# Optimization experiments

Hardware: AMD Instinct MI355X
Metric: run time of the kernel (lower is better)

## Reference

```python
import jax, jax.numpy as jnp
import numpy as np

B, L, D, H = 2, 4096, 1024, 4
DV = D // H
NP = 5
MIN_PROB = 0.01
CHUNK = 32
RIN = D + H * NP * 4 + H * (NP * (NP - 1)) // 2  # 1144
RH = 2 * RIN


def dwconv_causal(x, w):
    # x: (B, L, C); w: (C, K) depthwise causal FIR
    K = w.shape[-1]
    xp = jnp.pad(x, ((0, 0), (K - 1, 0), (0, 0))).transpose(0, 2, 1)  # (B,C,L+K-1)
    y = jax.lax.conv_general_dilated(
        xp, w[:, None, :], window_strides=(1,), padding='VALID',
        feature_group_count=w.shape[0],
        dimension_numbers=('NCH', 'OIH', 'NCH'))
    return y.transpose(0, 2, 1)  # (B,L,C)


def l2norm(x):
    return x * jax.lax.rsqrt(jnp.sum(x * x, -1, keepdims=True) + 1e-12)


def delta_rule_chunkwise(q, k, v, beta, chunk=CHUNK):
    # q,k: (b,h,L,dk)  v: (b,h,L,dv)  beta: (b,h,L); L divisible by chunk
    b, h, Lq, dk = q.shape
    dv = v.shape[-1]
    n = Lq // chunk
    q = l2norm(q); k = l2norm(k)
    v = v * beta[..., None]
    kb = k * beta[..., None]
    r = lambda x: x.reshape(b, h, n, chunk, -1)
    q, k, v, kb = r(q), r(k), r(v), r(kb)
    tri = jnp.triu(jnp.ones((chunk, chunk), bool), 0)
    attn = jnp.where(tri, 0.0, -(kb @ jnp.swapaxes(k, -1, -2)))
    for i in range(1, chunk):  # in-chunk triangular-inverse recurrence
        upd = jnp.einsum('...k,...ki->...i', attn[..., i, :], attn[..., :, :i])
        attn = attn.at[..., i, :i].add(upd)
    attn = attn + jnp.eye(chunk, dtype=attn.dtype)
    u = attn @ v
    w = attn @ kb
    strict = jnp.triu(jnp.ones((chunk, chunk), bool), 1)

    def step(S, inp):
        qi, ki, ui, wi = inp
        la = jnp.where(strict, 0.0, qi @ jnp.swapaxes(ki, -1, -2))
        u_i = ui - wi @ S
        o_i = qi @ S + la @ u_i
        return S + jnp.swapaxes(ki, -1, -2) @ u_i, o_i

    mv = lambda x: jnp.moveaxis(x, 2, 0)
    S0 = jnp.zeros((b, h, dk, dv), q.dtype)
    S, o = jax.lax.scan(step, S0, (mv(q), mv(k), mv(u), mv(w)))
    return jnp.moveaxis(o, 0, 2).reshape(b, h, Lq, dv), S


def setup_inputs() -> dict:
    key = jax.random.key(0)
    ks = jax.random.split(key, 20)
    f = lambda k, shape, s=0.02: jax.random.normal(k, shape, jnp.float32) * s
    # FIR filters: identity tap (last) + small noise, matching learned-from-delta init
    def fir(k, ksz):
        w = np.zeros((D, ksz), np.float32)
        w[:, -1] = 1.0
        return jnp.asarray(w) + f(k, (D, ksz), 0.02)
    b2 = np.zeros((H, NP), np.float32)
    b2[:, -1] = 0.5
    b2[:, -2] = 0.5
    return {
        'hidden_states': jax.random.normal(ks[0], (B, L, D), jnp.float32),
        'Wq': f(ks[1], (D, D)), 'Wk': f(ks[2], (D, D)), 'Wv': f(ks[3], (D, D)),
        'wq_conv': f(ks[4], (D, 4), 0.2), 'wk_conv': f(ks[5], (D, 4), 0.2),
        'wv_conv': f(ks[6], (D, 4), 0.2),
        'Wb': f(ks[7], (H, D)),
        'fir_s_w': fir(ks[8], 3), 'fir_m_w': fir(ks[9], 7),
        'fir_l_w': fir(ks[10], 25), 'fir_id_w': fir(ks[11], 1),
        'W1': f(ks[12], (RH, RIN)), 'b1': jnp.zeros((RH,), jnp.float32),
        'W2': f(ks[13], (H * NP, RH)), 'b2': jnp.asarray(b2.reshape(-1)),
        'norm_w': jnp.ones((DV,), jnp.float32),
        'Wo': f(ks[14], (D, D)),
    }


def reference(hidden_states, Wq, Wk, Wv, wq_conv, wk_conv, wv_conv, Wb,
              fir_s_w, fir_m_w, fir_l_w, fir_id_w, W1, b1, W2, b2, norm_w, Wo):
    silu = jax.nn.silu
    q = silu(dwconv_causal(hidden_states @ Wq.T, wq_conv))
    k = silu(dwconv_causal(hidden_states @ Wk.T, wk_conv))
    v = silu(dwconv_causal(hidden_states @ Wv.T, wv_conv))
    beta = jax.nn.sigmoid(hidden_states @ Wb.T)  # (B,L,H)
    q4 = q.reshape(B, L, H, -1).transpose(0, 2, 1, 3)
    k4 = k.reshape(B, L, H, -1).transpose(0, 2, 1, 3)
    v4 = v.reshape(B, L, H, -1).transpose(0, 2, 1, 3)
    delta_out, _ = delta_rule_chunkwise(q4, k4, v4, beta.transpose(0, 2, 1))
    delta_out = delta_out.transpose(0, 2, 1, 3)  # (B,L,H,DV)
    fir = lambda w: dwconv_causal(v, w).reshape(B, L, H, DV)
    branches = [fir(fir_s_w), fir(fir_m_w), fir(fir_l_w), delta_out, fir(fir_id_w)]
    feats = []
    for x in branches:
        sm = jax.nn.softmax(x, -1)
        feats += [x.mean(-1), jnp.var(x, -1, ddof=1), jnp.max(x, -1),
                  -(sm * jnp.log(sm + 1e-8)).sum(-1)]
    cross = []
    for i in range(NP):
        for j in range(i + 1, NP):
            xi, xj = branches[i], branches[j]
            den = jnp.sqrt(jnp.sum(xi * xi, -1)) * jnp.sqrt(jnp.sum(xj * xj, -1)) + 1e-8
            cross.append(jnp.sum(xi * xj, -1) / den)
    router_in = jnp.concatenate([hidden_states] + feats + cross, axis=-1)  # (B,L,RIN)
    hrt = jax.nn.gelu(router_in @ W1.T + b1, approximate=False)
    logits = (hrt @ W2.T + b2).reshape(B, L, H, NP)
    p = jax.nn.softmax(logits, -1)
    p = p * (1.0 - NP * MIN_PROB) + MIN_PROB  # probability floor
    out = jnp.einsum('blhp,pblhd->blhd', p, jnp.stack(branches))
    out = out * jax.lax.rsqrt(jnp.mean(out * out, -1, keepdims=True) + 1e-5) * norm_w
    return out.reshape(B, L, H * DV) @ Wo.T
```

## Files before the change

### kernel.cpp

```cpp
#include <hip/hip_runtime.h>
#include <stdint.h>

typedef unsigned short u16t;
typedef u16t us4 __attribute__((ext_vector_type(4)));
typedef u16t us8 __attribute__((ext_vector_type(8)));
typedef __bf16 bf8v __attribute__((ext_vector_type(8)));
typedef float f4 __attribute__((ext_vector_type(4)));

#define MFMA(a, b, c) __builtin_amdgcn_mfma_f32_16x16x32_bf16((a), (b), (c), 0, 0, 0)

__device__ __forceinline__ float bf2f(u16t u) {
  union { unsigned int i; float f; } c; c.i = ((unsigned int)u) << 16; return c.f;
}
__device__ __forceinline__ u16t f2bf(float f) {
  union { float f; unsigned int i; } c; c.f = f;
  return (u16t)((c.i + 0x7FFFu + ((c.i >> 16) & 1u)) >> 16);
}
__device__ __forceinline__ float wsum(float v) {
#pragma unroll
  for (int o = 32; o > 0; o >>= 1) v += __shfl_xor(v, o);
  return v;
}
__device__ __forceinline__ float wmax(float v) {
#pragma unroll
  for (int o = 32; o > 0; o >>= 1) v = fmaxf(v, __shfl_xor(v, o));
  return v;
}

__global__ __launch_bounds__(256) void pack_bf16(const float* __restrict__ src,
    u16t* __restrict__ dst, int n4) {
  const int i = blockIdx.x * 256 + threadIdx.x;
  if (i >= n4) return;
  f4 v = *(const f4*)&src[(size_t)i * 4];
  us4 o;
#pragma unroll
  for (int e = 0; e < 4; ++e) o[e] = f2bf(v[e]);
  *(us4*)&dst[(size_t)i * 4] = o;
}

template <bool AF32, bool BF32, bool CF32>
__device__ __forceinline__ void gemm_body(const void* __restrict__ Av,
    const void* __restrict__ Btv, void* __restrict__ Cv,
    int K, int lda, int ldb, int ldc, int m0, int n0) {
  __shared__ u16t As[128][40];
  __shared__ u16t Bs[128][40];
  const int tid = threadIdx.x;
  const int wv = tid >> 6, l = tid & 63;
  const int wr = wv >> 1, wc = wv & 1;
  const int lr = l & 15, kg8 = (l >> 4) * 8, rg4 = (l >> 4) * 4;
  const int row_s = tid >> 1, seg = (tid & 1) * 16;
  const f4 zf = {0.f, 0.f, 0.f, 0.f};
  f4 acc[4][4];
#pragma unroll
  for (int i = 0; i < 4; ++i)
#pragma unroll
    for (int j = 0; j < 4; ++j) acc[i][j] = zf;

  for (int kt = 0; kt < K; kt += 32) {
    us8 a0, a1, b0, b1;
    if (AF32) {
      const float* pa = (const float*)Av + (size_t)(m0 + row_s) * lda + seg + kt;
      f4 fa0 = *(const f4*)(pa), fa1 = *(const f4*)(pa + 4);
      f4 fa2 = *(const f4*)(pa + 8), fa3 = *(const f4*)(pa + 12);
#pragma unroll
      for (int e = 0; e < 4; ++e) {
// ... 21 lines not shown
    *(us8*)&As[row_s][seg + 8] = a1;
    *(us8*)&Bs[row_s][seg] = b0;
    *(us8*)&Bs[row_s][seg + 8] = b1;
    __syncthreads();
    bf8v af[4], bg[4];
#pragma unroll
    for (int f = 0; f < 4; ++f) af[f] = *(const bf8v*)&As[wr * 64 + f * 16 + lr][kg8];
#pragma unroll
    for (int f = 0; f < 4; ++f) bg[f] = *(const bf8v*)&Bs[wc * 64 + f * 16 + lr][kg8];
#pragma unroll
    for (int i = 0; i < 4; ++i)
#pragma unroll
      for (int j = 0; j < 4; ++j) acc[i][j] = MFMA(af[i], bg[j], acc[i][j]);
    __syncthreads();
  }
#pragma unroll
  for (int i = 0; i < 4; ++i) {
    const int rb = m0 + wr * 64 + i * 16 + rg4;
#pragma unroll
    for (int j = 0; j < 4; ++j) {
      const int cb = n0 + wc * 64 + j * 16 + lr;
#pragma unroll
      for (int r = 0; r < 4; ++r) {
        if (CF32)
          ((float*)Cv)[(size_t)(rb + r) * ldc + cb] = acc[i][j][r];
        else
          ((u16t*)Cv)[(size_t)(rb + r) * ldc + cb] = f2bf(acc[i][j][r]);
      }
    }
  }
}

template <bool AF32, bool BF32, bool CF32>
__global__ __launch_bounds__(256) void gemm_bt(const void* __restrict__ Av,
    const void* __restrict__ Btv, void* __restrict__ Cv,
    int K, int lda, int ldb, int ldc) {
  gemm_body<AF32, BF32, CF32>(Av, Btv, Cv, K, lda, ldb, ldc,
                              blockIdx.y * 128, blockIdx.x * 128);
}

__global__ __launch_bounds__(256) void gemm_qkv3(const u16t* __restrict__ A,
    const u16t* __restrict__ B0, const u16t* __restrict__ B1,
    const u16t* __restrict__ B2, u16t* __restrict__ C0, u16t* __restrict__ C1,
    u16t* __restrict__ C2v) {
  const int z = blockIdx.z;
  const u16t* Bt = (z == 0) ? B0 : ((z == 1) ? B1 : B2);
  u16t* C = (z == 0) ? C0 : ((z == 1) ? C1 : C2v);
  gemm_body<false, false, false>(A, Bt, C, 1024, 1024, 1024, 1024,
                                 blockIdx.y * 128, blockIdx.x * 128);
}

__global__ __launch_bounds__(256) void conv4_silu(
    const u16t* __restrict__ qlin, const u16t* __restrict__ klin, const u16t* __restrict__ vlin,
    const float* __restrict__ wq, const float* __restrict__ wk, const float* __restrict__ wvv,
    u16t* __restrict__ qc, u16t* __restrict__ kc, u16t* __restrict__ vc) {
  const int tid = threadIdx.x;
  const int l0 = blockIdx.x * 64;
  const int b = blockIdx.y >> 2, cb = blockIdx.y & 3;
  const int z = blockIdx.z;
  const u16t* in_ = (z == 0) ? qlin : ((z == 1) ? klin : vlin);
  const float* w_ = (z == 0) ? wq : ((z == 1) ? wk : wvv);
  u16t* out_ = (z == 0) ? qc : ((z == 1) ? kc : vc);
  const int c = cb * 256 + tid;
  __shared__ u16t sm[67][256];
  for (int i = 0; i < 67; ++i) {
    int ls = l0 - 3 + i;
    sm[i][tid] = (ls >= 0) ? in_[((size_t)b * 4096 + ls) * 1024 + c] : (u16t)0;
  }
  __syncthreads();
  f4 w4 = *(const f4*)&w_[c * 4];
  float x0 = bf2f(sm[0][tid]), x1 = bf2f(sm[1][tid]), x2 = bf2f(sm[2][tid]);
  for (int ll = 0; ll < 64; ++ll) {
    float x3 = bf2f(sm[ll + 3][tid]);
    float y = x0 * w4[0] + x1 * w4[1] + x2 * w4[2] + x3 * w4[3];
    y = y / (1.f + expf(-y));
    out_[((size_t)b * 4096 + l0 + ll) * 1024 + c] = f2bf(y);
    x0 = x1; x1 = x2; x2 = x3;
  }
}

__global__ __launch_bounds__(256) void beta_kernel(const float* __restrict__ hid,
    const float* __restrict__ Wb, float* __restrict__ beta) {
  const int m = blockIdx.x, tid = threadIdx.x;
  const int h = tid >> 6, l = tid & 63;
  float acc = 0.f;
#pragma unroll
  for (int it = 0; it < 4; ++it) {
    int kk = l * 4 + it * 256;
    f4 hv = *(const f4*)&hid[(size_t)m * 1024 + kk];
    f4 wv4 = *(const f4*)&Wb[(size_t)h * 1024 + kk];
#pragma unroll
    for (int e = 0; e < 4; ++e) acc += hv[e] * wv4[e];
  }
  acc = wsum(acc);
  if (l == 0) beta[m * 4 + h] = 1.f / (1.f + expf(-acc));
}

__global__ __launch_bounds__(256) void prep_kernel(u16t* __restrict__ qc, u16t* __restrict__ kc,
    const u16t* __restrict__ vc, const float* __restrict__ beta,
    u16t* __restrict__ kbeta, u16t* __restrict__ vbeta) {
  const int m = blockIdx.x, tid = threadIdx.x;
  const int h = tid >> 6, l = tid & 63;
  const size_t base = (size_t)m * 1024 + h * 256 + l * 4;
  const float bet = beta[m * 4 + h];
  us4 q4 = *(const us4*)&qc[base];
  float qf[4]; float ss = 0.f;
#pragma unroll
  for (int e = 0; e < 4; ++e) { qf[e] = bf2f(q4[e]); ss += qf[e] * qf[e]; }
  float qsc = rsqrtf(wsum(ss) + 1e-12f);
  us4 qo;
#pragma unroll
  for (int e = 0; e < 4; ++e) qo[e] = f2bf(qf[e] * qsc);
  *(us4*)&qc[base] = qo;
  us4 k4 = *(const us4*)&kc[base];
  float kf[4]; ss = 0.f;
#pragma unroll
  for (int e = 0; e < 4; ++e) { kf[e] = bf2f(k4[e]); ss += kf[e] * kf[e]; }
  float ksc = rsqrtf(wsum(ss) + 1e-12f);
  us4 ko, kbo;
#pragma unroll
  for (int e = 0; e < 4; ++e) {
    float kn = kf[e] * ksc;
    ko[e] = f2bf(kn);
    kbo[e] = f2bf(kn * bet);
  }
  *(us4*)&kc[base] = ko;
  *(us4*)&kbeta[base] = kbo;
// ... 74 lines not shown
        us8 v8 = *(const us8*)&vbs[j][cg + e0];
        us8 k8 = *(const us8*)&kbs[j][cg + e0];
#pragma unroll
        for (int e = 0; e < 8; ++e) {
          ua[e0 + e] += a * bf2f(v8[e]);
          wa[e0 + e] += a * bf2f(k8[e]);
        }
      }
    }
    const size_t ob = ((size_t)bh * 4096 + l0 + r) * 256 + cg;
#pragma unroll
    for (int e0 = 0; e0 < 32; e0 += 8) {
      us8 pu, pw;
#pragma unroll
      for (int e = 0; e < 8; ++e) { pu[e] = f2bf(ua[e0 + e]); pw[e] = f2bf(wa[e0 + e]); }
      *(us8*)&ug[ob + e0] = pu;
      *(us8*)&wg[ob + e0] = pw;
    }
  }
}

__global__ __launch_bounds__(256, 1) void delta_scan(const u16t* __restrict__ qn,
    const u16t* __restrict__ kn, const u16t* __restrict__ ug, const u16t* __restrict__ wg,
    u16t* __restrict__ dout) {
  const int blk = blockIdx.x;
  const int bh = blk >> 2, vbidx = blk & 3;
  const int b = bh >> 2, h = bh & 3;
  const int c0 = vbidx * 64;
  const int tid = threadIdx.x;
  const int wv = tid >> 6, l = tid & 63;
  const int lr = l & 15, kg8 = (l >> 4) * 8, rg4 = (l >> 4) * 4;

  __shared__ u16t qs[32][264], ks2[32][264], wss[32][264];
  __shared__ u16t kts[256][40];
  __shared__ u16t sbf[64][264];
  __shared__ u16t las[32][40];
  __shared__ u16t uts[64][40];

  {
    u16t* sp = &sbf[0][0];
    for (int i = tid; i < 64 * 264; i += 256) sp[i] = 0;
  }
  const f4 zf = {0.f, 0.f, 0.f, 0.f};
  f4 sacc[16];
#pragma unroll
  for (int d = 0; d < 16; ++d) sacc[d] = zf;
  __syncthreads();

  const u16t* qb = qn + (size_t)b * 4096 * 1024 + (size_t)h * 256;
  const u16t* knb = kn + (size_t)b * 4096 * 1024 + (size_t)h * 256;
  const u16t* ub = ug + (size_t)bh * 4096 * 256;
  const u16t* wb = wg + (size_t)bh * 4096 * 256;
  const int sr = tid >> 5, sd8 = (tid & 31) * 8;

  us8 pq[4], pk[4], pw[4];
  us4 pu0, pu1;
  {
#pragma unroll
    for (int i = 0; i < 4; ++i) {
      const int r = i * 8 + sr;
      pq[i] = *(const us8*)(qb + (size_t)r * 1024 + sd8);
      pk[i] = *(const us8*)(knb + (size_t)r * 1024 + sd8);
      pw[i] = *(const us8*)(wb + (size_t)r * 256 + sd8);
    }
    pu0 = *(const us4*)(ub + (size_t)lr * 256 + c0 + wv * 16 + rg4);
    pu1 = *(const us4*)(ub + (size_t)(16 + lr) * 256 + c0 + wv * 16 + rg4);
  }

  for (int ci = 0; ci < 128; ++ci) {
    const int l0 = ci * 32;
#pragma unroll
    for (int i = 0; i < 4; ++i) {
      const int r = i * 8 + sr;
      *(us8*)&qs[r][sd8] = pq[i];
      *(us8*)&ks2[r][sd8] = pk[i];
      *(us8*)&wss[r][sd8] = pw[i];
    }
    const us4 u0 = pu0, u1 = pu1;
    __syncthreads();
    if (ci < 127) {
      const int l1 = l0 + 32;
#pragma unroll
      for (int i = 0; i < 4; ++i) {
        const int r = i * 8 + sr;
        pq[i] = *(const us8*)(qb + (size_t)(l1 + r) * 1024 + sd8);
        pk[i] = *(const us8*)(knb + (size_t)(l1 + r) * 1024 + sd8);
        pw[i] = *(const us8*)(wb + (size_t)(l1 + r) * 256 + sd8);
      }
      pu0 = *(const us4*)(ub + (size_t)(l1 + lr) * 256 + c0 + wv * 16 + rg4);
      pu1 = *(const us4*)(ub + (size_t)(l1 + 16 + lr) * 256 + c0 + wv * 16 + rg4);
    }
    {
      const int dk = tid;
      const int swz = ((dk >> 3) & 3) << 3;
#pragma unroll
      for (int r = 0; r < 32; r += 2) {
        unsigned int lo = ks2[r][dk], hi = ks2[r + 1][dk];
        *(unsigned int*)&kts[dk][r ^ swz] = lo | (hi << 16);
      }
    }
    {
      const int rq = wv >> 1, rk = wv & 1;
      f4 t4 = zf;
#pragma unroll
      for (int ks = 0; ks < 8; ++ks) {
        bf8v a = *(const bf8v*)&qs[rq * 16 + lr][ks * 32 + kg8];
        bf8v bb = *(const bf8v*)&ks2[rk * 16 + lr][ks * 32 + kg8];
        t4 = MFMA(a, bb, t4);
      }
      const int colj = rk * 16 + lr;
#pragma unroll
      for (int rr = 0; rr < 4; ++rr) {
        const int rowr = rq * 16 + rg4 + rr;
        las[rowr][colj] = (colj <= rowr) ? f2bf(t4[rr]) : (u16t)0;
      }
    }
    f4 o0 = zf, o1 = zf;
    {
      f4 m0 = zf, m1 = zf;
#pragma unroll
      for (int ks = 0; ks < 8; ++ks) {
        bf8v a = *(const bf8v*)&sbf[wv * 16 + lr][ks * 32 + kg8];
        bf8v wb0 = *(const bf8v*)&wss[lr][ks * 32 + kg8];
        bf8v wb1 = *(const bf8v*)&wss[16 + lr][ks * 32 + kg8];
        bf8v qb0 = *(const bf8v*)&qs[lr][ks * 32 + kg8];
        bf8v qb1 = *(const bf8v*)&qs[16 + lr][ks * 32 + kg8];
        m0 = MFMA(a, wb0, m0);
        m1 = MFMA(a, wb1, m1);
        o0 = MFMA(a, qb0, o0);
        o1 = MFMA(a, qb1, o1);
      }
#pragma unroll
      for (int rt = 0; rt < 2; ++rt) {
        f4 mm = rt ? m1 : m0;
        const us4 uu = rt ? u1 : u0;
        const int r = rt * 16 + lr;
#pragma unroll
        for (int rr = 0; rr < 4; ++rr)
          uts[wv * 16 + rg4 + rr][r] = f2bf(bf2f(uu[rr]) - mm[rr]);
      }
    }
    __syncthreads();
    {
      bf8v a2 = *(const bf8v*)&uts[wv * 16 + lr][kg8];
      {
        bf8v lb0 = *(const bf8v*)&las[lr][kg8];
        bf8v lb1 = *(const bf8v*)&las[16 + lr][kg8];
        o0 = MFMA(a2, lb0, o0);
        o1 = MFMA(a2, lb1, o1);
      }
#pragma unroll
      for (int rt = 0; rt < 2; ++rt) {
        f4 oo = rt ? o1 : o0;
        const int r = rt * 16 + lr;
        us4 st;
#pragma unroll
        for (int rr = 0; rr < 4; ++rr) st[rr] = f2bf(oo[rr]);
        *(us4*)(dout + ((size_t)(b * 4096 + l0 + r) * 4 + h) * 256 + c0 + wv * 16 + rg4) = st;
      }
#pragma unroll
      for (int d = 0; d < 16; ++d) {
        const int swzd = ((2 * d + (lr >> 3)) & 3) << 3;
        bf8v bb = *(const bf8v*)&kts[d * 16 + lr][kg8 ^ swzd];
        sacc[d] = MFMA(a2, bb, sacc[d]);
      }
#pragma unroll
      for (int d = 0; d < 16; ++d) {
#pragma unroll
        for (int rr = 0; rr < 4; ++rr)
          sbf[wv * 16 + rg4 + rr][d * 16 + lr] = f2bf(sacc[d][rr]);
      }
    }
    __syncthreads();
  }
}

__global__ __launch_bounds__(256) void fir_kernel(const u16t* __restrict__ vc,
    const float* __restrict__ w3g, const float* __restrict__ w7g,
    const float* __restrict__ w25g, const float* __restrict__ w1g,
    u16t* __restrict__ fs, u16t* __restrict__ fm, u16t* __restrict__ fl,
    u16t* __restrict__ fid) {
  const int tid = threadIdx.x;
  const int l0 = blockIdx.x * 64;
  const int b = blockIdx.y >> 2, cb = blockIdx.y & 3;
  const int c = cb * 256 + tid;
  __shared__ u16t sm[88][256];
  for (int i = 0; i < 88; ++i) {
    int ls = l0 - 24 + i;
    sm[i][tid] = (ls >= 0) ? vc[((size_t)b * 4096 + ls) * 1024 + c] : (u16t)0;
  }
  __syncthreads();
  float w3[3], w7[7], w25[25], w1_;
#pragma unroll
  for (int j = 0; j < 3; ++j) w3[j] = w3g[c * 3 + j];
#pragma unroll
  for (int j = 0; j < 7; ++j) w7[j] = w7g[c * 7 + j];
#pragma unroll
  for (int j = 0; j < 25; ++j) w25[j] = w25g[c * 25 + j];
  w1_ = w1g[c];
  float x[25];
#pragma unroll
  for (int j = 0; j < 25; ++j) x[j] = bf2f(sm[j][tid]);
  for (int ll = 0; ll < 64; ++ll) {
    float ys = x[22] * w3[0] + x[23] * w3[1] + x[24] * w3[2];
    float ym = 0.f;
#pragma unroll
    for (int j = 0; j < 7; ++j) ym += x[18 + j] * w7[j];
    float yl = 0.f;
#pragma unroll
    for (int j = 0; j < 25; ++j) yl += x[j] * w25[j];
    float yi = x[24] * w1_;
    const size_t o = ((size_t)b * 4096 + l0 + ll) * 1024 + c;
    fs[o] = f2bf(ys); fm[o] = f2bf(ym); fl[o] = f2bf(yl); fid[o] = f2bf(yi);
    if (ll < 63) {
#pragma unroll
      for (int j = 0; j < 24; ++j) x[j] = x[j + 1];
      x[24] = bf2f(sm[ll + 25][tid]);
    }
  }
}

__global__ __launch_bounds__(256) void features_kernel(const float* __restrict__ hid,
    const u16t* __restrict__ p0, const u16t* __restrict__ p1, const u16t* __restrict__ p2,
    const u16t* __restrict__ p3, const u16t* __restrict__ p4, u16t* __restrict__ router) {
  const int m = blockIdx.x, tid = threadIdx.x;
  const int h = tid >> 6, l = tid & 63;
  const size_t base = (size_t)m * 1024 + h * 256 + l * 4;
  const u16t* bp[5] = {p0, p1, p2, p3, p4};
  float x[5][4];
#pragma unroll
  for (int br = 0; br < 5; ++br) {
    us4 v = *(const us4*)&bp[br][base];
#pragma unroll
    for (int e = 0; e < 4; ++e) x[br][e] = bf2f(v[e]);
  }
  float s1[5], s2[5], mx[5];
#pragma unroll
  for (int br = 0; br < 5; ++br) {
    float a = 0.f, bq = 0.f, m_ = -1e30f;
#pragma unroll
    for (int e = 0; e < 4; ++e) {
      a += x[br][e]; bq += x[br][e] * x[br][e]; m_ = fmaxf(m_, x[br][e]);
    }
    s1[br] = wsum(a); s2[br] = wsum(bq); mx[br] = wmax(m_);
  }
  float ent[5];
#pragma unroll
  for (int br = 0; br < 5; ++br) {
    float e_ = 0.f;
#pragma unroll
    for (int e = 0; e < 4; ++e) e_ += expf(x[br][e] - mx[br]);
    float es = wsum(e_);
    float hn = 0.f;
#pragma unroll
    for (int e = 0; e < 4; ++e) {
      float pv = expf(x[br][e] - mx[br]) / es;
      hn += pv * logf(pv + 1e-8f);
// ... 25 lines not shown
      rp[br * 16 + 8 + h] = f2bf(mx[br]);
      rp[br * 16 + 12 + h] = f2bf(ent[br]);
    }
    int pi = 0;
#pragma unroll
    for (int i = 0; i < 5; ++i)
#pragma unroll
      for (int j = i + 1; j < 5; ++j) {
        float den = sqrtf(s2[i]) * sqrtf(s2[j]) + 1e-8f;
        rp[80 + pi * 4 + h] = f2bf(dt[pi] / den);
        ++pi;
      }
  }
  {
    f4 hv = *(const f4*)&hid[(size_t)m * 1024 + tid * 4];
    us4 hv4;
#pragma unroll
    for (int e = 0; e < 4; ++e) hv4[e] = f2bf(hv[e]);
    *(us4*)&router[(size_t)m * 1152 + tid * 4] = hv4;
  }
  if (tid < 8) router[(size_t)m * 1152 + 1144 + tid] = 0;
}

__global__ __launch_bounds__(256) void gelu_bias(u16t* __restrict__ hrt,
    const float* __restrict__ b1) {
  const size_t idx = ((size_t)blockIdx.x * 256 + threadIdx.x) * 4;
  const int col = (int)(idx % 2304);
  us4 v = *(const us4*)&hrt[idx];
  us4 o;
#pragma unroll
  for (int e = 0; e < 4; ++e) {
    int cc = col + e;
    float xx = bf2f(v[e]) + ((cc < 2288) ? b1[cc] : 0.f);
    float g = 0.5f * xx * (1.f + erff(xx * 0.70710678118f));
    o[e] = f2bf(g);
  }
  *(us4*)&hrt[idx] = o;
}

__global__ __launch_bounds__(256) void w2_softmax(const u16t* __restrict__ hrt,
    const float* __restrict__ W2, const float* __restrict__ b2, float* __restrict__ pout) {
  const int m = blockIdx.x, tid = threadIdx.x;
  const int h = tid >> 6, l = tid & 63;
  float acc[5];
#pragma unroll
  for (int n = 0; n < 5; ++n) acc[n] = 0.f;
  for (int kk = l * 4; kk < 2288; kk += 256) {
    us4 hv = *(const us4*)&hrt[(size_t)m * 2304 + kk];
    float hf[4];
#pragma unroll
    for (int e = 0; e < 4; ++e) hf[e] = bf2f(hv[e]);
#pragma unroll
    for (int n = 0; n < 5; ++n) {
      f4 wv4 = *(const f4*)&W2[(size_t)(h * 5 + n) * 2288 + kk];
#pragma unroll
      for (int e = 0; e < 4; ++e) acc[n] += hf[e] * wv4[e];
    }
  }
#pragma unroll
  for (int n = 0; n < 5; ++n) acc[n] = wsum(acc[n]);
  if (l == 0) {
    float lg[5];
#pragma unroll
    for (int n = 0; n < 5; ++n) lg[n] = acc[n] + b2[h * 5 + n];
    float mxv = lg[0];
#pragma unroll
    for (int n = 1; n < 5; ++n) mxv = fmaxf(mxv, lg[n]);
    float es = 0.f, ev[5];
#pragma unroll
    for (int n = 0; n < 5; ++n) { ev[n] = expf(lg[n] - mxv); es += ev[n]; }
#pragma unroll
    for (int n = 0; n < 5; ++n)
      pout[(size_t)m * 20 + h * 5 + n] = (ev[n] / es) * 0.95f + 0.01f;
  }
}

__global__ __launch_bounds__(256) void mix_kernel(const u16t* __restrict__ p0,
    const u16t* __restrict__ p1, const u16t* __restrict__ p2, const u16t* __restrict__ p3,
    const u16t* __restrict__ p4, const float* __restrict__ pbuf,
    const float* __restrict__ normw, u16t* __restrict__ mixed) {
  const int m = blockIdx.x, tid = threadIdx.x;
  const int h = tid >> 6, l = tid & 63;
  const size_t base = (size_t)m * 1024 + h * 256 + l * 4;
  const u16t* bp[5] = {p0, p1, p2, p3, p4};
  float p5[5];
#pragma unroll
  for (int n = 0; n < 5; ++n) p5[n] = pbuf[(size_t)m * 20 + h * 5 + n];
  float o[4] = {0.f, 0.f, 0.f, 0.f};
#pragma unroll
  for (int br = 0; br < 5; ++br) {
    us4 v = *(const us4*)&bp[br][base];
#pragma unroll
    for (int e = 0; e < 4; ++e) o[e] += p5[br] * bf2f(v[e]);
  }
  float ss = 0.f;
#pragma unroll
  for (int e = 0; e < 4; ++e) ss += o[e] * o[e];
  ss = wsum(ss);
  float sc = rsqrtf(ss * (1.f / 256.f) + 1e-5f);
  f4 nw = *(const f4*)&normw[l * 4];
  us4 ov;
#pragma unroll
  for (int e = 0; e < 4; ++e) ov[e] = f2bf(o[e] * sc * nw[e]);
  *(us4*)&mixed[base] = ov;
}

__global__ __launch_bounds__(256) void pad_w1(const float* __restrict__ W1,
    u16t* __restrict__ W1p) {
  size_t idx = (size_t)blockIdx.x * 256 + threadIdx.x;
  if (idx >= (size_t)2304 * 1152) return;
  int n = (int)(idx / 1152), k = (int)(idx % 1152);
  W1p[idx] = (n < 2288 && k < 1144) ? f2bf(W1[(size_t)n * 1144 + k]) : (u16t)0;
}

extern "C" void kernel_launch(void* const* d_in, const int* in_sizes, int n_in,
                              void* d_out, int out_size, void* d_ws, size_t ws_size,
                              hipStream_t stream) {
  (void)in_sizes; (void)n_in; (void)out_size; (void)ws_size;
  const float* hid = (const float*)d_in[0];
  const float* Wq = (const float*)d_in[1];
  const float* Wk = (const float*)d_in[2];
  const float* Wv = (const float*)d_in[3];
  const float* wqc = (const float*)d_in[4];
  const float* wkc = (const float*)d_in[5];
  const float* wvc = (const float*)d_in[6];
  const float* Wb = (const float*)d_in[7];
  const float* fsw = (const float*)d_in[8];
  const float* fmw = (const float*)d_in[9];
  const float* flw = (const float*)d_in[10];
  const float* fiw = (const float*)d_in[11];
  const float* W1 = (const float*)d_in[12];
  const float* b1 = (const float*)d_in[13];
  const float* W2 = (const float*)d_in[14];
  const float* b2 = (const float*)d_in[15];
  const float* nwt = (const float*)d_in[16];
  const float* Wo = (const float*)d_in[17];
  float* out = (float*)d_out;

  char* wsp = (char*)d_ws;
  const size_t S = (size_t)2 * 4096 * 1024 * 2;
  u16t* ql = (u16t*)(wsp + 0 * S);
  u16t* kl = (u16t*)(wsp + 1 * S);
  u16t* vl = (u16t*)(wsp + 2 * S);
  u16t* qc = (u16t*)(wsp + 3 * S);
  u16t* kc = (u16t*)(wsp + 4 * S);
  u16t* vc = (u16t*)(wsp + 5 * S);
  u16t* ubuf = (u16t*)(wsp + 6 * S);
  u16t* wbuf = (u16t*)(wsp + 7 * S);
  char* p = wsp + 8 * S;
  u16t* router = (u16t*)p; p += (size_t)8192 * 1152 * 2;
  u16t* hrt = (u16t*)p;    p += (size_t)8192 * 2304 * 2;
  u16t* w1p = (u16t*)p;    p += (size_t)2304 * 1152 * 2;
  float* pbuf = (float*)p; p += (size_t)8192 * 20 * 4;
  float* beta = (float*)p; p += (size_t)8192 * 4 * 4;
  u16t* hidb = qc;
  u16t* wqb = kc;
  u16t* wkb = kc + 1048576;
  u16t* wvb = kc + 2097152;
  u16t* kbeta = ql;
  u16t* vbeta = kl;
  u16t* dlt = kl;
  u16t* f_s = vl;
  u16t* f_m = qc;
  u16t* f_l = kc;
  u16t* f_i = ubuf;
  u16t* mixed = wbuf;
  u16t* wob = w1p;

  dim3 blk(256);
  pack_bf16<<<dim3(8192), blk, 0, stream>>>(hid, hidb, 2097152);
  pack_bf16<<<dim3(1024), blk, 0, stream>>>(Wq, wqb, 262144);
  pack_bf16<<<dim3(1024), blk, 0, stream>>>(Wk, wkb, 262144);
  pack_bf16<<<dim3(1024), blk, 0, stream>>>(Wv, wvb, 262144);
  gemm_qkv3<<<dim3(8, 64, 3), blk, 0, stream>>>(hidb, wqb, wkb, wvb, ql, kl, vl);
  conv4_silu<<<dim3(64, 8, 3), blk, 0, stream>>>(ql, kl, vl, wqc, wkc, wvc, qc, kc, vc);
  beta_kernel<<<dim3(8192), blk, 0, stream>>>(hid, Wb, beta);
  prep_kernel<<<dim3(8192), blk, 0, stream>>>(qc, kc, vc, beta, kbeta, vbeta);
  chunk_uw<<<dim3(1024), blk, 0, stream>>>(kc, kbeta, vbeta, ubuf, wbuf);
  delta_scan<<<dim3(32), blk, 0, stream>>>(qc, kc, ubuf, wbuf, dlt);
  fir_kernel<<<dim3(64, 8), blk, 0, stream>>>(vc, fsw, fmw, flw, fiw, f_s, f_m, f_l, f_i);
  features_kernel<<<dim3(8192), blk, 0, stream>>>(hid, f_s, f_m, f_l, dlt, f_i, router);
  pad_w1<<<dim3(10368), blk, 0, stream>>>(W1, w1p);
  gemm_bt<false, false, false><<<dim3(18, 64), blk, 0, stream>>>(router, w1p, hrt, 1152, 1152, 1152, 2304);
  gelu_bias<<<dim3(18432), blk, 0, stream>>>(hrt, b1);
  w2_softmax<<<dim3(8192), blk, 0, stream>>>(hrt, W2, b2, pbuf);
  mix_kernel<<<dim3(8192), blk, 0, stream>>>(f_s, f_m, f_l, dlt, f_i, pbuf, nwt, mixed);
  pack_bf16<<<dim3(1024), blk, 0, stream>>>(Wo, wob, 262144);
  gemm_bt<false, false, true><<<dim3(8, 64), blk, 0, stream>>>(mixed, wob, out, 1024, 1024, 1024, 1024);
}
```

Measured before the change: 1.099 ms.

## Fuse packs, beta, gelu epilogue; overlap FIR and W1 pad with delta scan

Merges the four fp32-to-bf16 pack launches into one, folds beta computation into prep_kernel, and moves bias+GELU into the W1 GEMM epilogue, removing a full pass over hrt. The 32-block delta_scan launch now also carries extra blocks that compute the 25-tap FIR and pad W1, so that work uses otherwise idle CUs during the serial scan. Short FIRs (3, 7, identity) are recomputed on the fly in features and mix kernels instead of being stored. The cost is a larger delta_scan kernel with more shared memory and a risk of register and occupancy pressure, plus redundant FIR recompute in two kernels.

```diff
diff --git a/kernel.cpp b/kernel.cpp
--- a/kernel.cpp
+++ b/kernel.cpp
@@ -25,6 +25,23 @@
 #pragma unroll
   for (int o = 32; o > 0; o >>= 1) v = fmaxf(v, __shfl_xor(v, o));
   return v;
+}
+
+__global__ __launch_bounds__(256) void pack_all(const float* __restrict__ hid,
+    const float* __restrict__ Wq, const float* __restrict__ Wk, const float* __restrict__ Wv,
+    u16t* __restrict__ hidb, u16t* __restrict__ wqb, u16t* __restrict__ wkb,
+    u16t* __restrict__ wvb) {
+  const int g = blockIdx.x * 256 + threadIdx.x;
+  const float* src; u16t* dst; int off;
+  if (g < 2097152) { src = hid; dst = hidb; off = g; }
+  else if (g < 2359296) { src = Wq; dst = wqb; off = g - 2097152; }
+  else if (g < 2621440) { src = Wk; dst = wkb; off = g - 2359296; }
+  else { src = Wv; dst = wvb; off = g - 2621440; }
+  f4 v = *(const f4*)&src[(size_t)off * 4];
+  us4 o;
+#pragma unroll
+  for (int e = 0; e < 4; ++e) o[e] = f2bf(v[e]);
+  *(us4*)&dst[(size_t)off * 4] = o;
 }
 
 __global__ __launch_bounds__(256) void pack_bf16(const float* __restrict__ src,
@@ -38,9 +55,9 @@
   *(us4*)&dst[(size_t)i * 4] = o;
 }
 
-template <bool AF32, bool BF32, bool CF32>
+template <bool AF32, bool BF32, bool CF32, int EPI>
 __device__ __forceinline__ void gemm_body(const void* __restrict__ Av,
-    const void* __restrict__ Btv, void* __restrict__ Cv,
+    const void* __restrict__ Btv, void* __restrict__ Cv, const float* __restrict__ bias,
     int K, int lda, int ldb, int ldc, int m0, int n0) {
   __shared__ u16t As[128][40];
   __shared__ u16t Bs[128][40];
@@ -108,21 +125,26 @@
       const int cb = n0 + wc * 64 + j * 16 + lr;
 #pragma unroll
       for (int r = 0; r < 4; ++r) {
+        float x = acc[i][j][r];
+        if (EPI == 1) {
+          float xx = x + ((cb < 2288) ? bias[cb] : 0.f);
+          x = 0.5f * xx * (1.f + erff(xx * 0.70710678118f));
+        }
         if (CF32)
-          ((float*)Cv)[(size_t)(rb + r) * ldc + cb] = acc[i][j][r];
+          ((float*)Cv)[(size_t)(rb + r) * ldc + cb] = x;
         else
-          ((u16t*)Cv)[(size_t)(rb + r) * ldc + cb] = f2bf(acc[i][j][r]);
-      }
-    }
-  }
-}
-
-template <bool AF32, bool BF32, bool CF32>
+          ((u16t*)Cv)[(size_t)(rb + r) * ldc + cb] = f2bf(x);
+      }
+    }
+  }
+}
+
+template <bool AF32, bool BF32, bool CF32, int EPI>
 __global__ __launch_bounds__(256) void gemm_bt(const void* __restrict__ Av,
-    const void* __restrict__ Btv, void* __restrict__ Cv,
+    const void* __restrict__ Btv, void* __restrict__ Cv, const float* __restrict__ bias,
     int K, int lda, int ldb, int ldc) {
-  gemm_body<AF32, BF32, CF32>(Av, Btv, Cv, K, lda, ldb, ldc,
-                              blockIdx.y * 128, blockIdx.x * 128);
+  gemm_body<AF32, BF32, CF32, EPI>(Av, Btv, Cv, bias, K, lda, ldb, ldc,
+                                   blockIdx.y * 128, blockIdx.x * 128);
 }
 
 __global__ __launch_bounds__(256) void gemm_qkv3(const u16t* __restrict__ A,
@@ -132,8 +154,8 @@
   const int z = blockIdx.z;
   const u16t* Bt = (z == 0) ? B0 : ((z == 1) ? B1 : B2);
   u16t* C = (z == 0) ? C0 : ((z == 1) ? C1 : C2v);
-  gemm_body<false, false, false>(A, Bt, C, 1024, 1024, 1024, 1024,
-                                 blockIdx.y * 128, blockIdx.x * 128);
+  gemm_body<false, false, false, 0>(A, Bt, C, nullptr, 1024, 1024, 1024, 1024,
+                                    blockIdx.y * 128, blockIdx.x * 128);
 }
 
 __global__ __launch_bounds__(256) void conv4_silu(
@@ -165,30 +187,22 @@
   }
 }
 
-__global__ __launch_bounds__(256) void beta_kernel(const float* __restrict__ hid,
-    const float* __restrict__ Wb, float* __restrict__ beta) {
+__global__ __launch_bounds__(256) void prep_kernel(u16t* __restrict__ qc, u16t* __restrict__ kc,
+    const u16t* __restrict__ vc, const float* __restrict__ hid, const float* __restrict__ Wb,
+    u16t* __restrict__ kbeta, u16t* __restrict__ vbeta) {
   const int m = blockIdx.x, tid = threadIdx.x;
   const int h = tid >> 6, l = tid & 63;
-  float acc = 0.f;
+  float bacc = 0.f;
 #pragma unroll
   for (int it = 0; it < 4; ++it) {
     int kk = l * 4 + it * 256;
     f4 hv = *(const f4*)&hid[(size_t)m * 1024 + kk];
     f4 wv4 = *(const f4*)&Wb[(size_t)h * 1024 + kk];
 #pragma unroll
-    for (int e = 0; e < 4; ++e) acc += hv[e] * wv4[e];
-  }
-  acc = wsum(acc);
-  if (l == 0) beta[m * 4 + h] = 1.f / (1.f + expf(-acc));
-}
-
-__global__ __launch_bounds__(256) void prep_kernel(u16t* __restrict__ qc, u16t* __restrict__ kc,
-    const u16t* __restrict__ vc, const float* __restrict__ beta,
-    u16t* __restrict__ kbeta, u16t* __restrict__ vbeta) {
-  const int m = blockIdx.x, tid = threadIdx.x;
-  const int h = tid >> 6, l = tid & 63;
+    for (int e = 0; e < 4; ++e) bacc += hv[e] * wv4[e];
+  }
+  const float bet = 1.f / (1.f + expf(-wsum(bacc)));
   const size_t base = (size_t)m * 1024 + h * 256 + l * 4;
-  const float bet = beta[m * 4 + h];
   us4 q4 = *(const us4*)&qc[base];
   float qf[4]; float ss = 0.f;
 #pragma unroll
@@ -309,40 +323,41 @@
 
 __global__ __launch_bounds__(256, 1) void delta_scan(const u16t* __restrict__ qn,
     const u16t* __restrict__ kn, const u16t* __restrict__ ug, const u16t* __restrict__ wg,
-    u16t* __restrict__ dout) {
+    u16t* __restrict__ dout, const u16t* __restrict__ vc, const float* __restrict__ w25g,
+    u16t* __restrict__ fl, const float* __restrict__ W1, u16t* __restrict__ W1p) {
   const int blk = blockIdx.x;
-  const int bh = blk >> 2, vbidx = blk & 3;
-  const int b = bh >> 2, h = bh & 3;
-  const int c0 = vbidx * 64;
   const int tid = threadIdx.x;
-  const int wv = tid >> 6, l = tid & 63;
-  const int lr = l & 15, kg8 = (l >> 4) * 8, rg4 = (l >> 4) * 4;
-
-  __shared__ u16t qs[32][264], ks2[32][264], wss[32][264];
-  __shared__ u16t kts[256][40];
-  __shared__ u16t sbf[64][264];
-  __shared__ u16t las[32][40];
-  __shared__ u16t uts[64][40];
-
-  {
-    u16t* sp = &sbf[0][0];
-    for (int i = tid; i < 64 * 264; i += 256) sp[i] = 0;
-  }
-  const f4 zf = {0.f, 0.f, 0.f, 0.f};
-  f4 sacc[16];
-#pragma unroll
-  for (int d = 0; d < 16; ++d) sacc[d] = zf;
-  __syncthreads();
-
-  const u16t* qb = qn + (size_t)b * 4096 * 1024 + (size_t)h * 256;
-  const u16t* knb = kn + (size_t)b * 4096 * 1024 + (size_t)h * 256;
-  const u16t* ub = ug + (size_t)bh * 4096 * 256;
-  const u16t* wb = wg + (size_t)bh * 4096 * 256;
-  const int sr = tid >> 5, sd8 = (tid & 31) * 8;
-
-  us8 pq[4], pk[4], pw[4];
-  us4 pu0, pu1;
-  {
+  if (blk < 32) {
+    const int bh = blk >> 2, vbidx = blk & 3;
+    const int b = bh >> 2, h = bh & 3;
+    const int c0 = vbidx * 64;
+    const int wv = tid >> 6, l = tid & 63;
+    const int lr = l & 15, kg8 = (l >> 4) * 8, rg4 = (l >> 4) * 4;
+
+    __shared__ u16t qs[32][264], ks2[32][264], wss[32][264];
+    __shared__ u16t kts[256][40];
+    __shared__ u16t sbf[64][264];
+    __shared__ u16t las[32][40];
+    __shared__ u16t uts[64][40];
+
+    {
+      u16t* sp = &sbf[0][0];
+      for (int i = tid; i < 64 * 264; i += 256) sp[i] = 0;
+    }
+    const f4 zf = {0.f, 0.f, 0.f, 0.f};
+    f4 sacc[16];
+#pragma unroll
+    for (int d = 0; d < 16; ++d) sacc[d] = zf;
+    __syncthreads();
+
+    const u16t* qb = qn + (size_t)b * 4096 * 1024 + (size_t)h * 256;
+    const u16t* knb = kn + (size_t)b * 4096 * 1024 + (size_t)h * 256;
+    const u16t* ub = ug + (size_t)bh * 4096 * 256;
+    const u16t* wb = wg + (size_t)bh * 4096 * 256;
+    const int sr = tid >> 5, sd8 = (tid & 31) * 8;
+
+    us8 pq[4], pk[4], pw[4];
+    us4 pu0, pu1;
 #pragma unroll
     for (int i = 0; i < 4; ++i) {
       const int r = i * 8 + sr;
@@ -352,174 +367,198 @@
     }
     pu0 = *(const us4*)(ub + (size_t)lr * 256 + c0 + wv * 16 + rg4);
     pu1 = *(const us4*)(ub + (size_t)(16 + lr) * 256 + c0 + wv * 16 + rg4);
-  }
-
-  for (int ci = 0; ci < 128; ++ci) {
-    const int l0 = ci * 32;
-#pragma unroll
-    for (int i = 0; i < 4; ++i) {
-      const int r = i * 8 + sr;
-      *(us8*)&qs[r][sd8] = pq[i];
-      *(us8*)&ks2[r][sd8] = pk[i];
-      *(us8*)&wss[r][sd8] = pw[i];
-    }
-    const us4 u0 = pu0, u1 = pu1;
-    __syncthreads();
-    if (ci < 127) {
-      const int l1 = l0 + 32;
+
+    for (int ci = 0; ci < 128; ++ci) {
+      const int l0 = ci * 32;
 #pragma unroll
       for (int i = 0; i < 4; ++i) {
         const int r = i * 8 + sr;
-        pq[i] = *(const us8*)(qb + (size_t)(l1 + r) * 1024 + sd8);
-        pk[i] = *(const us8*)(knb + (size_t)(l1 + r) * 1024 + sd8);
-        pw[i] = *(const us8*)(wb + (size_t)(l1 + r) * 256 + sd8);
-      }
-      pu0 = *(const us4*)(ub + (size_t)(l1 + lr) * 256 + c0 + wv * 16 + rg4);
-      pu1 = *(const us4*)(ub + (size_t)(l1 + 16 + lr) * 256 + c0 + wv * 16 + rg4);
-    }
-    {
-      const int dk = tid;
-      const int swz = ((dk >> 3) & 3) << 3;
-#pragma unroll
-      for (int r = 0; r < 32; r += 2) {
-        unsigned int lo = ks2[r][dk], hi = ks2[r + 1][dk];
-        *(unsigned int*)&kts[dk][r ^ swz] = lo | (hi << 16);
-      }
-    }
-    {
-      const int rq = wv >> 1, rk = wv & 1;
-      f4 t4 = zf;
-#pragma unroll
-      for (int ks = 0; ks < 8; ++ks) {
-        bf8v a = *(const bf8v*)&qs[rq * 16 + lr][ks * 32 + kg8];
-        bf8v bb = *(const bf8v*)&ks2[rk * 16 + lr][ks * 32 + kg8];
-        t4 = MFMA(a, bb, t4);
-      }
-      const int colj = rk * 16 + lr;
-#pragma unroll
-      for (int rr = 0; rr < 4; ++rr) {
-        const int rowr = rq * 16 + rg4 + rr;
-        las[rowr][colj] = (colj <= rowr) ? f2bf(t4[rr]) : (u16t)0;
-      }
-    }
-    f4 o0 = zf, o1 = zf;
-    {
-      f4 m0 = zf, m1 = zf;
-#pragma unroll
-      for (int ks = 0; ks < 8; ++ks) {
-        bf8v a = *(const bf8v*)&sbf[wv * 16 + lr][ks * 32 + kg8];
-        bf8v wb0 = *(const bf8v*)&wss[lr][ks * 32 + kg8];
-        bf8v wb1 = *(const bf8v*)&wss[16 + lr][ks * 32 + kg8];
-        bf8v qb0 = *(const bf8v*)&qs[lr][ks * 32 + kg8];
-        bf8v qb1 = *(const bf8v*)&qs[16 + lr][ks * 32 + kg8];
-        m0 = MFMA(a, wb0, m0);
-        m1 = MFMA(a, wb1, m1);
-        o0 = MFMA(a, qb0, o0);
-        o1 = MFMA(a, qb1, o1);
-      }
-#pragma unroll
-      for (int rt = 0; rt < 2; ++rt) {
-        f4 mm = rt ? m1 : m0;
-        const us4 uu = rt ? u1 : u0;
-        const int r = rt * 16 + lr;
-#pragma unroll
-        for (int rr = 0; rr < 4; ++rr)
-          uts[wv * 16 + rg4 + rr][r] = f2bf(bf2f(uu[rr]) - mm[rr]);
-      }
+        *(us8*)&qs[r][sd8] = pq[i];
+        *(us8*)&ks2[r][sd8] = pk[i];
+        *(us8*)&wss[r][sd8] = pw[i];
+      }
+      const us4 u0 = pu0, u1 = pu1;
+      __syncthreads();
+      if (ci < 127) {
+        const int l1 = l0 + 32;
+#pragma unroll
+        for (int i = 0; i < 4; ++i) {
+          const int r = i * 8 + sr;
+          pq[i] = *(const us8*)(qb + (size_t)(l1 + r) * 1024 + sd8);
+          pk[i] = *(const us8*)(knb + (size_t)(l1 + r) * 1024 + sd8);
+          pw[i] = *(const us8*)(wb + (size_t)(l1 + r) * 256 + sd8);
+        }
+        pu0 = *(const us4*)(ub + (size_t)(l1 + lr) * 256 + c0 + wv * 16 + rg4);
+        pu1 = *(const us4*)(ub + (size_t)(l1 + 16 + lr) * 256 + c0 + wv * 16 + rg4);
+      }
+      {
+        const int dk = tid;
+        const int swz = ((dk >> 3) & 3) << 3;
+#pragma unroll
+        for (int r = 0; r < 32; r += 2) {
+          unsigned int lo = ks2[r][dk], hi = ks2[r + 1][dk];
+          *(unsigned int*)&kts[dk][r ^ swz] = lo | (hi << 16);
+        }
+      }
+      {
+        const int rq = wv >> 1, rk = wv & 1;
+        f4 t4 = zf;
+#pragma unroll
+        for (int ks = 0; ks < 8; ++ks) {
+          bf8v a = *(const bf8v*)&qs[rq * 16 + lr][ks * 32 + kg8];
+          bf8v bb = *(const bf8v*)&ks2[rk * 16 + lr][ks * 32 + kg8];
+          t4 = MFMA(a, bb, t4);
+        }
+        const int colj = rk * 16 + lr;
+#pragma unroll
+        for (int rr = 0; rr < 4; ++rr) {
+          const int rowr = rq * 16 + rg4 + rr;
+          las[rowr][colj] = (colj <= rowr) ? f2bf(t4[rr]) : (u16t)0;
+        }
+      }
+      f4 o0 = zf, o1 = zf;
+      {
+        f4 m0 = zf, m1 = zf;
+#pragma unroll
+        for (int ks = 0; ks < 8; ++ks) {
+          bf8v a = *(const bf8v*)&sbf[wv * 16 + lr][ks * 32 + kg8];
+          bf8v wb0 = *(const bf8v*)&wss[lr][ks * 32 + kg8];
+          bf8v wb1 = *(const bf8v*)&wss[16 + lr][ks * 32 + kg8];
+          bf8v qb0 = *(const bf8v*)&qs[lr][ks * 32 + kg8];
+          bf8v qb1 = *(const bf8v*)&qs[16 + lr][ks * 32 + kg8];
+          m0 = MFMA(a, wb0, m0);
+          m1 = MFMA(a, wb1, m1);
+          o0 = MFMA(a, qb0, o0);
+          o1 = MFMA(a, qb1, o1);
+        }
+#pragma unroll
+        for (int rt = 0; rt < 2; ++rt) {
+          f4 mm = rt ? m1 : m0;
+          const us4 uu = rt ? u1 : u0;
+          const int r = rt * 16 + lr;
+#pragma unroll
+          for (int rr = 0; rr < 4; ++rr)
+            uts[wv * 16 + rg4 + rr][r] = f2bf(bf2f(uu[rr]) - mm[rr]);
+        }
+      }
+      __syncthreads();
+      {
+        bf8v a2 = *(const bf8v*)&uts[wv * 16 + lr][kg8];
+        {
+          bf8v lb0 = *(const bf8v*)&las[lr][kg8];
+          bf8v lb1 = *(const bf8v*)&las[16 + lr][kg8];
+          o0 = MFMA(a2, lb0, o0);
+          o1 = MFMA(a2, lb1, o1);
+        }
+#pragma unroll
+        for (int rt = 0; rt < 2; ++rt) {
+          f4 oo = rt ? o1 : o0;
+          const int r = rt * 16 + lr;
+          us4 st;
+#pragma unroll
+          for (int rr = 0; rr < 4; ++rr) st[rr] = f2bf(oo[rr]);
+          *(us4*)(dout + ((size_t)(b * 4096 + l0 + r) * 4 + h) * 256 + c0 + wv * 16 + rg4) = st;
+        }
+#pragma unroll
+        for (int d = 0; d < 16; ++d) {
+          const int swzd = ((2 * d + (lr >> 3)) & 3) << 3;
+          bf8v bb = *(const bf8v*)&kts[d * 16 + lr][kg8 ^ swzd];
+          sacc[d] = MFMA(a2, bb, sacc[d]);
+        }
+#pragma unroll
+        for (int d = 0; d < 16; ++d) {
+#pragma unroll
+          for (int rr = 0; rr < 4; ++rr)
+            sbf[wv * 16 + rg4 + rr][d * 16 + lr] = f2bf(sacc[d][rr]);
+        }
+      }
+      __syncthreads();
+    }
+    return;
+  }
+  if (blk < 544) {
+    const int fb = blk - 32;
+    const int l0 = (fb & 63) * 64;
+    const int by = fb >> 6;
+    const int b = by >> 2, cb = by & 3;
+    const int c = cb * 256 + tid;
+    __shared__ u16t sm[88][256];
+    for (int i = 0; i < 88; ++i) {
+      int ls = l0 - 24 + i;
+      sm[i][tid] = (ls >= 0) ? vc[((size_t)b * 4096 + ls) * 1024 + c] : (u16t)0;
     }
     __syncthreads();
-    {
-      bf8v a2 = *(const bf8v*)&uts[wv * 16 + lr][kg8];
-      {
-        bf8v lb0 = *(const bf8v*)&las[lr][kg8];
-        bf8v lb1 = *(const bf8v*)&las[16 + lr][kg8];
-        o0 = MFMA(a2, lb0, o0);
-        o1 = MFMA(a2, lb1, o1);
-      }
-#pragma unroll
-      for (int rt = 0; rt < 2; ++rt) {
-        f4 oo = rt ? o1 : o0;
-        const int r = rt * 16 + lr;
-        us4 st;
-#pragma unroll
-        for (int rr = 0; rr < 4; ++rr) st[rr] = f2bf(oo[rr]);
-        *(us4*)(dout + ((size_t)(b * 4096 + l0 + r) * 4 + h) * 256 + c0 + wv * 16 + rg4) = st;
-      }
-#pragma unroll
-      for (int d = 0; d < 16; ++d) {
-        const int swzd = ((2 * d + (lr >> 3)) & 3) << 3;
-        bf8v bb = *(const bf8v*)&kts[d * 16 + lr][kg8 ^ swzd];
-        sacc[d] = MFMA(a2, bb, sacc[d]);
-      }
-#pragma unroll
-      for (int d = 0; d < 16; ++d) {
-#pragma unroll
-        for (int rr = 0; rr < 4; ++rr)
-          sbf[wv * 16 + rg4 + rr][d * 16 + lr] = f2bf(sacc[d][rr]);
-      }
-    }
-    __syncthreads();
-  }
-}
-
-__global__ __launch_bounds__(256) void fir_kernel(const u16t* __restrict__ vc,
+    float w25[25];
+#pragma unroll
+    for (int j = 0; j < 25; ++j) w25[j] = w25g[c * 25 + j];
+    float x[25];
+#pragma unroll
+    for (int j = 0; j < 25; ++j) x[j] = bf2f(sm[j][tid]);
+    for (int ll = 0; ll < 64; ++ll) {
+      float yl = 0.f;
+#pragma unroll
+      for (int j = 0; j < 25; ++j) yl += x[j] * w25[j];
+      fl[((size_t)b * 4096 + l0 + ll) * 1024 + c] = f2bf(yl);
+      if (ll < 63) {
+#pragma unroll
+        for (int j = 0; j < 24; ++j) x[j] = x[j + 1];
+        x[24] = bf2f(sm[ll + 25][tid]);
+      }
+    }
+    return;
+  }
+  for (size_t idx = (size_t)(blk - 544) * 256 + tid; idx < (size_t)2304 * 1152;
+       idx += (size_t)128 * 256) {
+    int n = (int)(idx / 1152), k = (int)(idx % 1152);
+    W1p[idx] = (n < 2288 && k < 1144) ? f2bf(W1[(size_t)n * 1144 + k]) : (u16t)0;
+  }
+}
+
+__device__ __forceinline__ void fir_otf(const u16t* __restrict__ vc,
     const float* __restrict__ w3g, const float* __restrict__ w7g,
-    const float* __restrict__ w25g, const float* __restrict__ w1g,
-    u16t* __restrict__ fs, u16t* __restrict__ fm, u16t* __restrict__ fl,
-    u16t* __restrict__ fid) {
-  const int tid = threadIdx.x;
-  const int l0 = blockIdx.x * 64;
-  const int b = blockIdx.y >> 2, cb = blockIdx.y & 3;
-  const int c = cb * 256 + tid;
-  __shared__ u16t sm[88][256];
-  for (int i = 0; i < 88; ++i) {
-    int ls = l0 - 24 + i;
-    sm[i][tid] = (ls >= 0) ? vc[((size_t)b * 4096 + ls) * 1024 + c] : (u16t)0;
-  }
-  __syncthreads();
-  float w3[3], w7[7], w25[25], w1_;
-#pragma unroll
-  for (int j = 0; j < 3; ++j) w3[j] = w3g[c * 3 + j];
-#pragma unroll
-  for (int j = 0; j < 7; ++j) w7[j] = w7g[c * 7 + j];
-#pragma unroll
-  for (int j = 0; j < 25; ++j) w25[j] = w25g[c * 25 + j];
-  w1_ = w1g[c];
-  float x[25];
-#pragma unroll
-  for (int j = 0; j < 25; ++j) x[j] = bf2f(sm[j][tid]);
-  for (int ll = 0; ll < 64; ++ll) {
-    float ys = x[22] * w3[0] + x[23] * w3[1] + x[24] * w3[2];
-    float ym = 0.f;
-#pragma unroll
-    for (int j = 0; j < 7; ++j) ym += x[18 + j] * w7[j];
-    float yl = 0.f;
-#pragma unroll
-    for (int j = 0; j < 25; ++j) yl += x[j] * w25[j];
-    float yi = x[24] * w1_;
-    const size_t o = ((size_t)b * 4096 + l0 + ll) * 1024 + c;
-    fs[o] = f2bf(ys); fm[o] = f2bf(ym); fl[o] = f2bf(yl); fid[o] = f2bf(yi);
-    if (ll < 63) {
-#pragma unroll
-      for (int j = 0; j < 24; ++j) x[j] = x[j + 1];
-      x[24] = bf2f(sm[ll + 25][tid]);
-    }
+    const float* __restrict__ w1g, int b, int lseq, int c0,
+    float ys[4], float ym[4], float yi[4]) {
+  float xs[7][4];
+#pragma unroll
+  for (int j = 0; j < 7; ++j) {
+    int ls = lseq - 6 + j;
+    if (ls >= 0) {
+      us4 v = *(const us4*)&vc[((size_t)b * 4096 + ls) * 1024 + c0];
+#pragma unroll
+      for (int e = 0; e < 4; ++e) xs[j][e] = bf2f(v[e]);
+    } else {
+#pragma unroll
+      for (int e = 0; e < 4; ++e) xs[j][e] = 0.f;
+    }
+  }
+#pragma unroll
+  for (int e = 0; e < 4; ++e) {
+    const int c = c0 + e;
+    ys[e] = xs[4][e] * w3g[c * 3] + xs[5][e] * w3g[c * 3 + 1] + xs[6][e] * w3g[c * 3 + 2];
+    float m_ = 0.f;
+#pragma unroll
+    for (int j = 0; j < 7; ++j) m_ += xs[j][e] * w7g[c * 7 + j];
+    ym[e] = m_;
+    yi[e] = xs[6][e] * w1g[c];
   }
 }
 
 __global__ __launch_bounds__(256) void features_kernel(const float* __restrict__ hid,
-    const u16t* __restrict__ p0, const u16t* __restrict__ p1, const u16t* __restrict__ p2,
-    const u16t* __restrict__ p3, const u16t* __restrict__ p4, u16t* __restrict__ router) {
+    const u16t* __restrict__ vc, const float* __restrict__ w3g, const float* __restrict__ w7g,
+    const float* __restrict__ w1g, const u16t* __restrict__ fl, const u16t* __restrict__ dlt,
+    u16t* __restrict__ router) {
   const int m = blockIdx.x, tid = threadIdx.x;
   const int h = tid >> 6, l = tid & 63;
-  const size_t base = (size_t)m * 1024 + h * 256 + l * 4;
-  const u16t* bp[5] = {p0, p1, p2, p3, p4};
+  const int b = m >> 12, lseq = m & 4095;
+  const int c0 = h * 256 + l * 4;
+  const size_t base = (size_t)m * 1024 + c0;
   float x[5][4];
-#pragma unroll
-  for (int br = 0; br < 5; ++br) {
-    us4 v = *(const us4*)&bp[br][base];
-#pragma unroll
-    for (int e = 0; e < 4; ++e) x[br][e] = bf2f(v[e]);
+  fir_otf(vc, w3g, w7g, w1g, b, lseq, c0, x[0], x[1], x[4]);
+  {
+    us4 v2 = *(const us4*)&fl[base];
+    us4 v3 = *(const us4*)&dlt[base];
+#pragma unroll
+    for (int e = 0; e < 4; ++e) { x[2][e] = bf2f(v2[e]); x[3][e] = bf2f(v3[e]); }
   }
   float s1[5], s2[5], mx[5];
 #pragma unroll
@@ -591,22 +630,6 @@
   if (tid < 8) router[(size_t)m * 1152 + 1144 + tid] = 0;
 }
 
-__global__ __launch_bounds__(256) void gelu_bias(u16t* __restrict__ hrt,
-    const float* __restrict__ b1) {
-  const size_t idx = ((size_t)blockIdx.x * 256 + threadIdx.x) * 4;
-  const int col = (int)(idx % 2304);
-  us4 v = *(const us4*)&hrt[idx];
-  us4 o;
-#pragma unroll
-  for (int e = 0; e < 4; ++e) {
-    int cc = col + e;
-    float xx = bf2f(v[e]) + ((cc < 2288) ? b1[cc] : 0.f);
-    float g = 0.5f * xx * (1.f + erff(xx * 0.70710678118f));
-    o[e] = f2bf(g);
-  }
-  *(us4*)&hrt[idx] = o;
-}
-
 __global__ __launch_bounds__(256) void w2_softmax(const u16t* __restrict__ hrt,
     const float* __restrict__ W2, const float* __restrict__ b2, float* __restrict__ pout) {
   const int m = blockIdx.x, tid = threadIdx.x;
@@ -644,24 +667,32 @@
   }
 }
 
-__global__ __launch_bounds__(256) void mix_kernel(const u16t* __restrict__ p0,
-    const u16t* __restrict__ p1, const u16t* __restrict__ p2, const u16t* __restrict__ p3,
-    const u16t* __restrict__ p4, const float* __restrict__ pbuf,
+__global__ __launch_bounds__(256) void mix_kernel(const u16t* __restrict__ vc,
+    const float* __restrict__ w3g, const float* __restrict__ w7g,
+    const float* __restrict__ w1g, const u16t* __restrict__ fl,
+    const u16t* __restrict__ dlt, const float* __restrict__ pbuf,
     const float* __restrict__ normw, u16t* __restrict__ mixed) {
   const int m = blockIdx.x, tid = threadIdx.x;
   const int h = tid >> 6, l = tid & 63;
-  const size_t base = (size_t)m * 1024 + h * 256 + l * 4;
-  const u16t* bp[5] = {p0, p1, p2, p3, p4};
+  const int b = m >> 12, lseq = m & 4095;
+  const int c0 = h * 256 + l * 4;
+  const size_t base = (size_t)m * 1024 + c0;
+  float x[5][4];
+  fir_otf(vc, w3g, w7g, w1g, b, lseq, c0, x[0], x[1], x[4]);
+  {
+    us4 v2 = *(const us4*)&fl[base];
+    us4 v3 = *(const us4*)&dlt[base];
+#pragma unroll
+    for (int e = 0; e < 4; ++e) { x[2][e] = bf2f(v2[e]); x[3][e] = bf2f(v3[e]); }
+  }
   float p5[5];
 #pragma unroll
   for (int n = 0; n < 5; ++n) p5[n] = pbuf[(size_t)m * 20 + h * 5 + n];
   float o[4] = {0.f, 0.f, 0.f, 0.f};
 #pragma unroll
-  for (int br = 0; br < 5; ++br) {
-    us4 v = *(const us4*)&bp[br][base];
-#pragma unroll
-    for (int e = 0; e < 4; ++e) o[e] += p5[br] * bf2f(v[e]);
-  }
+  for (int br = 0; br < 5; ++br)
+#pragma unroll
+    for (int e = 0; e < 4; ++e) o[e] += p5[br] * x[br][e];
   float ss = 0.f;
 #pragma unroll
   for (int e = 0; e < 4; ++e) ss += o[e] * o[e];
@@ -672,14 +703,6 @@
 #pragma unroll
   for (int e = 0; e < 4; ++e) ov[e] = f2bf(o[e] * sc * nw[e]);
   *(us4*)&mixed[base] = ov;
-}
-
-__global__ __launch_bounds__(256) void pad_w1(const float* __restrict__ W1,
-    u16t* __restrict__ W1p) {
-  size_t idx = (size_t)blockIdx.x * 256 + threadIdx.x;
-  if (idx >= (size_t)2304 * 1152) return;
-  int n = (int)(idx / 1152), k = (int)(idx % 1152);
-  W1p[idx] = (n < 2288 && k < 1144) ? f2bf(W1[(size_t)n * 1144 + k]) : (u16t)0;
 }
 
 extern "C" void kernel_launch(void* const* d_in, const int* in_sizes, int n_in,
@@ -721,7 +744,6 @@
   u16t* hrt = (u16t*)p;    p += (size_t)8192 * 2304 * 2;
   u16t* w1p = (u16t*)p;    p += (size_t)2304 * 1152 * 2;
   float* pbuf = (float*)p; p += (size_t)8192 * 20 * 4;
-  float* beta = (float*)p; p += (size_t)8192 * 4 * 4;
   u16t* hidb = qc;
   u16t* wqb = kc;
   u16t* wkb = kc + 1048576;
@@ -729,31 +751,21 @@
   u16t* kbeta = ql;
   u16t* vbeta = kl;
   u16t* dlt = kl;
-  u16t* f_s = vl;
-  u16t* f_m = qc;
-  u16t* f_l = kc;
-  u16t* f_i = ubuf;
+  u16t* f_l = vl;
   u16t* mixed = wbuf;
   u16t* wob = w1p;
 
   dim3 blk(256);
-  pack_bf16<<<dim3(8192), blk, 0, stream>>>(hid, hidb, 2097152);
-  pack_bf16<<<dim3(1024), blk, 0, stream>>>(Wq, wqb, 262144);
-  pack_bf16<<<dim3(1024), blk, 0, stream>>>(Wk, wkb, 262144);
-  pack_bf16<<<dim3(1024), blk, 0, stream>>>(Wv, wvb, 262144);
+  pack_all<<<dim3(11264), blk, 0, stream>>>(hid, Wq, Wk, Wv, hidb, wqb, wkb, wvb);
   gemm_qkv3<<<dim3(8, 64, 3), blk, 0, stream>>>(hidb, wqb, wkb, wvb, ql, kl, vl);
   conv4_silu<<<dim3(64, 8, 3), blk, 0, stream>>>(ql, kl, vl, wqc, wkc, wvc, qc, kc, vc);
-  beta_kernel<<<dim3(8192), blk, 0, stream>>>(hid, Wb, beta);
-  prep_kernel<<<dim3(8192), blk, 0, stream>>>(qc, kc, vc, beta, kbeta, vbeta);
+  prep_kernel<<<dim3(8192), blk, 0, stream>>>(qc, kc, vc, hid, Wb, kbeta, vbeta);
   chunk_uw<<<dim3(1024), blk, 0, stream>>>(kc, kbeta, vbeta, ubuf, wbuf);
-  delta_scan<<<dim3(32), blk, 0, stream>>>(qc, kc, ubuf, wbuf, dlt);
-  fir_kernel<<<dim3(64, 8), blk, 0, stream>>>(vc, fsw, fmw, flw, fiw, f_s, f_m, f_l, f_i);
-  features_kernel<<<dim3(8192), blk, 0, stream>>>(hid, f_s, f_m, f_l, dlt, f_i, router);
-  pad_w1<<<dim3(10368), blk, 0, stream>>>(W1, w1p);
-  gemm_bt<false, false, false><<<dim3(18, 64), blk, 0, stream>>>(router, w1p, hrt, 1152, 1152, 1152, 2304);
-  gelu_bias<<<dim3(18432), blk, 0, stream>>>(hrt, b1);
+  delta_scan<<<dim3(672), blk, 0, stream>>>(qc, kc, ubuf, wbuf, dlt, vc, flw, f_l, W1, w1p);
+  features_kernel<<<dim3(8192), blk, 0, stream>>>(hid, vc, fsw, fmw, fiw, f_l, dlt, router);
+  gemm_bt<false, false, false, 1><<<dim3(18, 64), blk, 0, stream>>>(router, w1p, hrt, b1, 1152, 1152, 1152, 2304);
   w2_softmax<<<dim3(8192), blk, 0, stream>>>(hrt, W2, b2, pbuf);
-  mix_kernel<<<dim3(8192), blk, 0, stream>>>(f_s, f_m, f_l, dlt, f_i, pbuf, nwt, mixed);
+  mix_kernel<<<dim3(8192), blk, 0, stream>>>(vc, fsw, fmw, fiw, f_l, dlt, pbuf, nwt, mixed);
   pack_bf16<<<dim3(1024), blk, 0, stream>>>(Wo, wob, 262144);
-  gemm_bt<false, false, true><<<dim3(8, 64), blk, 0, stream>>>(mixed, wob, out, 1024, 1024, 1024, 1024);
-}
+  gemm_bt<false, false, true, 0><<<dim3(8, 64), blk, 0, stream>>>(mixed, wob, out, nullptr, 1024, 1024, 1024, 1024);
+}
```

After: 1.078 ms. Within noise of the previous version (-1.9%).
